# Kernel tuning notes

Measured on AMD Instinct MI355X. Metric: run time of the kernel, lower is better.

The kernel has to match this reference:

```python
import jax, jax.numpy as jnp
import numpy as np

N = 100000
E = 3200000
F_IN = 512
H = 16
C = 40


def gcn_conv(x, edge_index, W, b, num_nodes):
    """PyG GCNConv: y = D^{-1/2} (A + I) D^{-1/2} (x @ W) + b.
    edge_index: [2, E] int, row=source, col=target; self-loops added here."""
    # transform first (small hidden dim keeps message traffic low)
    h = x @ W  # [N, out]
    loops = jnp.arange(num_nodes, dtype=edge_index.dtype)
    row = jnp.concatenate([edge_index[0], loops])
    col = jnp.concatenate([edge_index[1], loops])
    deg = jax.ops.segment_sum(jnp.ones_like(col, dtype=h.dtype), col,
                              num_segments=num_nodes)  # in-degree incl. self-loop
    dinv = jnp.where(deg > 0, jax.lax.rsqrt(deg), 0.0)
    norm = dinv[row] * dinv[col]  # [E+N]
    msgs = h[row] * norm[:, None]  # gather + scale, [E+N, out]
    out = jax.ops.segment_sum(msgs, col, num_segments=num_nodes)  # scatter-add
    return out + b


def setup_inputs() -> dict:
    key = jax.random.key(0)
    k1, k2, k3, k4, k5, k6 = jax.random.split(key, 6)
    x = jax.random.normal(k1, (N, F_IN), dtype=jnp.float32)
    edge_index = jax.random.randint(k2, (2, E), 0, N, dtype=jnp.int64)
    s1 = 1.0 / np.sqrt(F_IN)
    s2 = 1.0 / np.sqrt(H)
    W1 = jax.random.uniform(k3, (F_IN, H), jnp.float32, -s1, s1)
    b1 = jnp.zeros((H,), jnp.float32)
    W2 = jax.random.uniform(k4, (H, C), jnp.float32, -s2, s2)
    b2 = jnp.zeros((C,), jnp.float32)
    return {"x": x, "edge_index": edge_index, "W1": W1, "b1": b1,
            "W2": W2, "b2": b2}


def reference(x, edge_index, W1, b1, W2, b2):
    h = gcn_conv(x, edge_index, W1, b1, N)
    h = jax.nn.relu(h)
    # F.dropout(training=self.training): inference mode -> identity
    h = gcn_conv(h, edge_index, W2, b2, N)
    return jax.nn.log_softmax(h, axis=1)
```

## Files before the change

### kernel.cpp

```cpp
#include <hip/hip_runtime.h>

#define NN 100000
#define EE 3200000
#define FIN 512
#define HH 16
#define CC 40

#define SHIFT 9
#define BNODES 512
#define NB 196
#define CAP 20480
#define CH 2048
#define TC ((EE + CH - 1) / CH)
#define GB ((NN * 4 + 255) / 256)
#define GB2 ((NN + 63) / 64)

__device__ __forceinline__ float bf2f(unsigned short u) {
    return __uint_as_float(((unsigned)u) << 16);
}
__device__ __forceinline__ unsigned short f2bf(float f) {
    unsigned b = __float_as_uint(f);
    return (unsigned short)((b + 0x7FFF + ((b >> 16) & 1)) >> 16);
}

__global__ void k_bin(const int* __restrict__ ei, int* __restrict__ head,
                      unsigned* __restrict__ pairs) {
    __shared__ int h[NB];
    __shared__ int gbase[NB];
    __shared__ int lhead[NB];
    __shared__ int is64_s;
    int t = threadIdx.x;
    if (t < 64) {
        int nz = (ei[2 * t + 1] != 0) ? 1 : 0;
        unsigned long long m = __ballot(nz);
        if (t == 0) is64_s = (m == 0ULL) ? 1 : 0;
    }
    for (int i = t; i < NB; i += 256) { h[i] = 0; lhead[i] = 0; }
    __syncthreads();
    int is64 = is64_s;
    int e0 = blockIdx.x * CH;
    unsigned es[8], ed[8];
#pragma unroll
    for (int j = 0; j < 8; ++j) {
        int e = e0 + j * 256 + t;
        if (e < EE) {
            es[j] = (unsigned)(is64 ? ei[2 * e] : ei[e]);
            ed[j] = (unsigned)(is64 ? ei[2 * (EE + e)] : ei[EE + e]);
            atomicAdd(&h[ed[j] >> SHIFT], 1);
        }
    }
    __syncthreads();
    for (int i = t; i < NB; i += 256)
        gbase[i] = h[i] ? atomicAdd(&head[i], h[i]) : 0;
    __syncthreads();
#pragma unroll
    for (int j = 0; j < 8; ++j) {
        int e = e0 + j * 256 + t;
        if (e < EE) {
            int b = (int)(ed[j] >> SHIFT);
            int p = gbase[b] + atomicAdd(&lhead[b], 1);
            pairs[(size_t)b * CAP + p] = ((ed[j] & (BNODES - 1)) << 17) | es[j];
        }
    }
}

__global__ void __launch_bounds__(256) k_buildgemm(
        const unsigned* __restrict__ pairs, const int* __restrict__ head,
        int* __restrict__ ptr, int* __restrict__ pend,
        float* __restrict__ dinv, int* __restrict__ srcs,
        const float* __restrict__ x, const float* __restrict__ W1,
        float* __restrict__ g1f) {
    __shared__ float red[4][64][17];
    int t = threadIdx.x;
    if (blockIdx.x < NB) {
        int* h   = (int*)red;
        int* lex = (int*)red + BNODES;
        int* wsm = (int*)red + 2 * BNODES;
        int b = blockIdx.x, lane = t & 63, wid = t >> 6;
        int node0 = b << SHIFT;
        int p0 = b * CAP;
        int cnt = head[b];
        for (int i = t; i < BNODES; i += 256) h[i] = 0;
        __syncthreads();
        for (int p = t; p < cnt; p += 256) atomicAdd(&h[pairs[p0 + p] >> 17], 1);
        __syncthreads();
        int a0 = h[2 * t], a1 = h[2 * t + 1];
        int s = a0 + a1;
        int v = s;
#pragma unroll
        for (int off = 1; off < 64; off <<= 1) {
            int u = __shfl_up(v, off);
            if (lane >= off) v += u;
        }
        if (lane == 63) wsm[wid] = v;
        __syncthreads();
        int add = 0;
        for (int w = 0; w < wid; ++w) add += wsm[w];
        int incl = v + add;
        int e0 = incl - s;
        lex[2 * t] = e0;
        lex[2 * t + 1] = e0 + a0;
        __syncthreads();
        for (int i = t; i < BNODES; i += 256) {
            int n = node0 + i;
            if (n < NN) {
                int st = p0 + lex[i];
                ptr[n] = st;
                pend[n] = st + h[i];
                dinv[n] = rsqrtf((float)(h[i] + 1));
            }
        }
        __syncthreads();
        for (int p = t; p < cnt; p += 256) {
            unsigned w = pairs[p0 + p];
            int pos = p0 + atomicAdd(&lex[w >> 17], 1);
            srcs[pos] = (int)(w & 0x1FFFF);
        }
    } else {
        int kq = __builtin_amdgcn_readfirstlane(t >> 6);
        int n = t & 63;
        int base = (blockIdx.x - NB) * 64;
        int nc = min(base + n, NN - 1);
        const float4* xr = reinterpret_cast<const float4*>(
            x + (size_t)nc * FIN + kq * 128);
        const float* wb = W1 + kq * 128 * HH;
        float acc[HH];
#pragma unroll
        for (int f = 0; f < HH; ++f) acc[f] = 0.f;
#pragma unroll 2
        for (int i = 0; i < 32; ++i) {
            float4 xv = xr[i];
            const float* wr = wb + i * 4 * HH;
#pragma unroll
            for (int f = 0; f < HH; ++f) acc[f] = fmaf(xv.x, wr[f], acc[f]);
#pragma unroll
            for (int f = 0; f < HH; ++f) acc[f] = fmaf(xv.y, wr[HH + f], acc[f]);
#pragma unroll
            for (int f = 0; f < HH; ++f) acc[f] = fmaf(xv.z, wr[2 * HH + f], acc[f]);
#pragma unroll
            for (int f = 0; f < HH; ++f) acc[f] = fmaf(xv.w, wr[3 * HH + f], acc[f]);
        }
#pragma unroll
        for (int f = 0; f < HH; ++f) red[kq][n][f] = acc[f];
        __syncthreads();
        int g = t >> 6;
        int f0 = g * 4;
        float r0 = red[0][n][f0]     + red[1][n][f0]     + red[2][n][f0]     + red[3][n][f0];
        float r1 = red[0][n][f0 + 1] + red[1][n][f0 + 1] + red[2][n][f0 + 1] + red[3][n][f0 + 1];
        float r2 = red[0][n][f0 + 2] + red[1][n][f0 + 2] + red[2][n][f0 + 2] + red[3][n][f0 + 2];
        float r3 = red[0][n][f0 + 3] + red[1][n][f0 + 3] + red[2][n][f0 + 3] + red[3][n][f0 + 3];
        int node = base + n;
        if (node < NN)
            reinterpret_cast<float4*>(g1f)[node * 4 + g] =
                make_float4(r0, r1, r2, r3);
    }
}

__global__ void k_scale(const float* __restrict__ g1f, const float* __restrict__ dinv,
                        unsigned short* __restrict__ g1) {
    int gt = blockIdx.x * 256 + threadIdx.x;
    int node = gt >> 2, q = gt & 3;
    if (node >= NN) return;
    float di = dinv[node];
    float4 v = reinterpret_cast<const float4*>(g1f)[node * 4 + q];
    ushort4 o;
    o.x = f2bf(v.x * di);
    o.y = f2bf(v.y * di);
    o.z = f2bf(v.z * di);
    o.w = f2bf(v.w * di);
    reinterpret_cast<ushort4*>(g1)[node * 4 + q] = o;
}

__global__ void k_agg1(const unsigned short* __restrict__ g1, const int* __restrict__ ptr,
                       const int* __restrict__ pend, const int* __restrict__ srcs,
                       const float* __restrict__ dinv, const float* __restrict__ b1,
                       unsigned short* __restrict__ g2h) {
    int gt = blockIdx.x * blockDim.x + threadIdx.x;
    int node = gt >> 2, q = gt & 3;
    if (node >= NN) return;
    const ushort4* G = reinterpret_cast<const ushort4*>(g1);
    ushort4 sv = G[node * 4 + q];
    float ax = bf2f(sv.x), ay = bf2f(sv.y), az = bf2f(sv.z), aw = bf2f(sv.w);
    float bx = 0.f, by = 0.f, bz = 0.f, bw = 0.f;
    float cx = 0.f, cy = 0.f, cz = 0.f, cw = 0.f;
    float dx = 0.f, dy = 0.f, dz = 0.f, dw = 0.f;
    int e = ptr[node], e1 = pend[node];
    for (; e + 3 < e1; e += 4) {
        int s0 = srcs[e], s1 = srcs[e + 1], s2 = srcs[e + 2], s3 = srcs[e + 3];
        ushort4 v0 = G[s0 * 4 + q];
        ushort4 v1 = G[s1 * 4 + q];
        ushort4 v2 = G[s2 * 4 + q];
        ushort4 v3 = G[s3 * 4 + q];
        ax += bf2f(v0.x); ay += bf2f(v0.y); az += bf2f(v0.z); aw += bf2f(v0.w);
        bx += bf2f(v1.x); by += bf2f(v1.y); bz += bf2f(v1.z); bw += bf2f(v1.w);
        cx += bf2f(v2.x); cy += bf2f(v2.y); cz += bf2f(v2.z); cw += bf2f(v2.w);
        dx += bf2f(v3.x); dy += bf2f(v3.y); dz += bf2f(v3.z); dw += bf2f(v3.w);
    }
    for (; e < e1; ++e) {
        ushort4 v = G[srcs[e] * 4 + q];
        ax += bf2f(v.x); ay += bf2f(v.y); az += bf2f(v.z); aw += bf2f(v.w);
    }
    ax += bx + cx + dx;
    ay += by + cy + dy;
    az += bz + cz + dz;
    aw += bw + cw + dw;
    float di = dinv[node];
    const float4 bb = reinterpret_cast<const float4*>(b1)[q];
    ushort4 r;
    r.x = f2bf(fmaxf(fmaf(di, ax, bb.x), 0.f) * di);
    r.y = f2bf(fmaxf(fmaf(di, ay, bb.y), 0.f) * di);
    r.z = f2bf(fmaxf(fmaf(di, az, bb.z), 0.f) * di);
    r.w = f2bf(fmaxf(fmaf(di, aw, bb.w), 0.f) * di);
    reinterpret_cast<ushort4*>(g2h)[node * 4 + q] = r;
}

__global__ void __launch_bounds__(256) k_agg2out(
        const unsigned short* __restrict__ g2h, const int* __restrict__ ptr,
        const int* __restrict__ pend, const int* __restrict__ srcs,
        const float* __restrict__ dinv, const float* __restrict__ W2,
        const float* __restrict__ b2, float* __restrict__ out) {
    __shared__ float w2s[HH * 41];
    __shared__ float b2s[CC];
    int t = threadIdx.x;
    for (int i = t; i < HH * CC; i += 256) w2s[(i / CC) * 41 + (i % CC)] = W2[i];
    if (t < CC) b2s[t] = b2[t];
    __syncthreads();
    int gt = blockIdx.x * blockDim.x + t;
    int node = gt >> 2, q = gt & 3;
    if (node >= NN) return;
    const ushort4* G = reinterpret_cast<const ushort4*>(g2h);
    ushort4 sv = G[node * 4 + q];
    float ax = bf2f(sv.x), ay = bf2f(sv.y), az = bf2f(sv.z), aw = bf2f(sv.w);
    float bx = 0.f, by = 0.f, bz = 0.f, bw = 0.f;
    float cx = 0.f, cy = 0.f, cz = 0.f, cw = 0.f;
    float dx = 0.f, dy = 0.f, dz = 0.f, dw = 0.f;
    int e = ptr[node], e1 = pend[node];
    for (; e + 3 < e1; e += 4) {
        int s0 = srcs[e], s1 = srcs[e + 1], s2 = srcs[e + 2], s3 = srcs[e + 3];
        ushort4 v0 = G[s0 * 4 + q];
        ushort4 v1 = G[s1 * 4 + q];
        ushort4 v2 = G[s2 * 4 + q];
        ushort4 v3 = G[s3 * 4 + q];
        ax += bf2f(v0.x); ay += bf2f(v0.y); az += bf2f(v0.z); aw += bf2f(v0.w);
        bx += bf2f(v1.x); by += bf2f(v1.y); bz += bf2f(v1.z); bw += bf2f(v1.w);
        cx += bf2f(v2.x); cy += bf2f(v2.y); cz += bf2f(v2.z); cw += bf2f(v2.w);
        dx += bf2f(v3.x); dy += bf2f(v3.y); dz += bf2f(v3.z); dw += bf2f(v3.w);
    }
    for (; e < e1; ++e) {
        ushort4 v = G[srcs[e] * 4 + q];
        ax += bf2f(v.x); ay += bf2f(v.y); az += bf2f(v.z); aw += bf2f(v.w);
    }
    ax += bx + cx + dx;
    ay += by + cy + dy;
    az += bz + cz + dz;
    aw += bw + cw + dw;
    const float* w0 = w2s + (4 * q + 0) * 41;
    const float* w1 = w2s + (4 * q + 1) * 41;
    const float* w2r = w2s + (4 * q + 2) * 41;
    const float* w3 = w2s + (4 * q + 3) * 41;
    float y[CC];
#pragma unroll
    for (int c = 0; c < CC; ++c)
        y[c] = fmaf(ax, w0[c], fmaf(ay, w1[c], fmaf(az, w2r[c], aw * w3[c])));
#pragma unroll
    for (int c = 0; c < CC; ++c) {
        y[c] += __shfl_xor(y[c], 1);
        y[c] += __shfl_xor(y[c], 2);
    }
    float di = dinv[node];
    float m = -3.0e38f;
#pragma unroll
    for (int c = 0; c < CC; ++c) {
        y[c] = fmaf(di, y[c], b2s[c]);
        m = fmaxf(m, y[c]);
    }
    float ssum = 0.f;
#pragma unroll
    for (int c = 0; c < CC; ++c) ssum += expf(y[c] - m);
    float l = logf(ssum) + m;
    float ov[10];
#pragma unroll
    for (int c = 0; c < CC; ++c) {
        if ((c / 10) == q) ov[c % 10] = y[c] - l;
    }
    float2* o2 = reinterpret_cast<float2*>(out + (size_t)node * CC + 10 * q);
#pragma unroll
    for (int i = 0; i < 5; ++i) o2[i] = make_float2(ov[2 * i], ov[2 * i + 1]);
}

extern "C" void kernel_launch(void* const* d_in, const int* in_sizes, int n_in,
                              void* d_out, int out_size, void* d_ws, size_t ws_size,
                              hipStream_t stream) {
    const float* x  = (const float*)d_in[0];
    const int*   ei = (const int*)d_in[1];
    const float* W1 = (const float*)d_in[2];
    const float* b1 = (const float*)d_in[3];
    const float* W2 = (const float*)d_in[4];
    const float* b2 = (const float*)d_in[5];
    float* out = (float*)d_out;

    char* w = (char*)d_ws;
    auto alloc = [&](size_t bytes) {
        char* p = w;
        w += (bytes + 255) & ~(size_t)255;
        return p;
    };
    int*            head  = (int*)alloc((size_t)NB * 4);
    int*            ptr   = (int*)alloc((size_t)NN * 4);
    int*            pend  = (int*)alloc((size_t)NN * 4);
    float*          dinv  = (float*)alloc((size_t)NN * 4);
    unsigned*       pairs = (unsigned*)alloc((size_t)NB * CAP * 4);
    int*            srcs  = (int*)alloc((size_t)NB * CAP * 4);
    float*          g1f   = (float*)alloc((size_t)NN * HH * 4);
    unsigned short* g1    = (unsigned short*)alloc((size_t)NN * HH * 2);
    unsigned short* g2h   = (unsigned short*)alloc((size_t)NN * HH * 2);

    hipMemsetAsync(head, 0, (size_t)NB * sizeof(int), stream);
    k_bin<<<TC, 256, 0, stream>>>(ei, head, pairs);
    k_buildgemm<<<NB + GB2, 256, 0, stream>>>(pairs, head, ptr, pend, dinv, srcs,
                                              x, W1, g1f);
    k_scale<<<GB, 256, 0, stream>>>(g1f, dinv, g1);
    int nt = NN * 4;
    k_agg1<<<(nt + 255) / 256, 256, 0, stream>>>(g1, ptr, pend, srcs, dinv, b1, g2h);
    k_agg2out<<<(nt + 255) / 256, 256, 0, stream>>>(g2h, ptr, pend, srcs, dinv,
                                                    W2, b2, out);
}
```

Measured before the change: 468.3 us.

## Stage x tiles through double-buffered swizzled LDS for coalesced GEMM loads

The x@W1 part of the fused build/GEMM kernel now loads x rows cooperatively and coalesced: eight lanes read 128 contiguous bytes of a row. The rows go into a double-buffered, XOR-swizzled shared-memory tile. Each wave then computes 4 output features for all 64 nodes, so the cross-wave LDS reduction of partial sums goes away. Previously each lane streamed its own row with strided float4 loads. The change adds a barrier per chunk and needs more LDS traffic, but it targets the uncoalesced global reads of the 200 MB x matrix.

```diff
diff --git a/kernel.cpp b/kernel.cpp
--- a/kernel.cpp
+++ b/kernel.cpp
@@ -70,12 +70,12 @@
         float* __restrict__ dinv, int* __restrict__ srcs,
         const float* __restrict__ x, const float* __restrict__ W1,
         float* __restrict__ g1f) {
-    __shared__ float red[4][64][17];
+    __shared__ float xs[2][64][32];
     int t = threadIdx.x;
     if (blockIdx.x < NB) {
-        int* h   = (int*)red;
-        int* lex = (int*)red + BNODES;
-        int* wsm = (int*)red + 2 * BNODES;
+        int* h   = (int*)xs;
+        int* lex = (int*)xs + BNODES;
+        int* wsm = (int*)xs + 2 * BNODES;
         int b = blockIdx.x, lane = t & 63, wid = t >> 6;
         int node0 = b << SHIFT;
         int p0 = b * CAP;
@@ -117,42 +117,63 @@
             srcs[pos] = (int)(w & 0x1FFFF);
         }
     } else {
-        int kq = __builtin_amdgcn_readfirstlane(t >> 6);
-        int n = t & 63;
+        int w = __builtin_amdgcn_readfirstlane(t >> 6);
+        int lane = t & 63;
+        int ln7 = lane & 7;
         int base = (blockIdx.x - NB) * 64;
-        int nc = min(base + n, NN - 1);
-        const float4* xr = reinterpret_cast<const float4*>(
-            x + (size_t)nc * FIN + kq * 128);
-        const float* wb = W1 + kq * 128 * HH;
-        float acc[HH];
-#pragma unroll
-        for (int f = 0; f < HH; ++f) acc[f] = 0.f;
-#pragma unroll 2
-        for (int i = 0; i < 32; ++i) {
-            float4 xv = xr[i];
-            const float* wr = wb + i * 4 * HH;
-#pragma unroll
-            for (int f = 0; f < HH; ++f) acc[f] = fmaf(xv.x, wr[f], acc[f]);
-#pragma unroll
-            for (int f = 0; f < HH; ++f) acc[f] = fmaf(xv.y, wr[HH + f], acc[f]);
-#pragma unroll
-            for (int f = 0; f < HH; ++f) acc[f] = fmaf(xv.z, wr[2 * HH + f], acc[f]);
-#pragma unroll
-            for (int f = 0; f < HH; ++f) acc[f] = fmaf(xv.w, wr[3 * HH + f], acc[f]);
-        }
-#pragma unroll
-        for (int f = 0; f < HH; ++f) red[kq][n][f] = acc[f];
-        __syncthreads();
-        int g = t >> 6;
-        int f0 = g * 4;
-        float r0 = red[0][n][f0]     + red[1][n][f0]     + red[2][n][f0]     + red[3][n][f0];
-        float r1 = red[0][n][f0 + 1] + red[1][n][f0 + 1] + red[2][n][f0 + 1] + red[3][n][f0 + 1];
-        float r2 = red[0][n][f0 + 2] + red[1][n][f0 + 2] + red[2][n][f0 + 2] + red[3][n][f0 + 2];
-        float r3 = red[0][n][f0 + 3] + red[1][n][f0 + 3] + red[2][n][f0 + 3] + red[3][n][f0 + 3];
-        int node = base + n;
+        int r0 = w * 16 + (lane >> 3);
+        int r1 = r0 + 8;
+        const float* src0 = x + (size_t)min(base + r0, NN - 1) * FIN + ln7 * 4;
+        const float* src1 = x + (size_t)min(base + r1, NN - 1) * FIN + ln7 * 4;
+        int c0 = (ln7 ^ (r0 & 7)) * 4;
+        int c1 = (ln7 ^ (r1 & 7)) * 4;
+        const float* wq = W1 + w * 4;
+        float4 acc = make_float4(0.f, 0.f, 0.f, 0.f);
+        {
+            float4 v0 = *(const float4*)(src0);
+            float4 v1 = *(const float4*)(src1);
+            *(float4*)&xs[0][r0][c0] = v0;
+            *(float4*)&xs[0][r1][c1] = v1;
+        }
+        __syncthreads();
+#pragma unroll 4
+        for (int ch = 0; ch < 16; ++ch) {
+            int cb = ch & 1;
+            float4 n0, n1;
+            if (ch < 15) {
+                n0 = *(const float4*)(src0 + (ch + 1) * 32);
+                n1 = *(const float4*)(src1 + (ch + 1) * 32);
+            }
+#pragma unroll
+            for (int s = 0; s < 8; ++s) {
+                float4 xv = *(const float4*)&xs[cb][lane][(s ^ ln7) * 4];
+                const float* wr = wq + (ch * 32 + s * 4) * HH;
+                acc.x = fmaf(xv.x, wr[0], acc.x);
+                acc.y = fmaf(xv.x, wr[1], acc.y);
+                acc.z = fmaf(xv.x, wr[2], acc.z);
+                acc.w = fmaf(xv.x, wr[3], acc.w);
+                acc.x = fmaf(xv.y, wr[HH + 0], acc.x);
+                acc.y = fmaf(xv.y, wr[HH + 1], acc.y);
+                acc.z = fmaf(xv.y, wr[HH + 2], acc.z);
+                acc.w = fmaf(xv.y, wr[HH + 3], acc.w);
+                acc.x = fmaf(xv.z, wr[2 * HH + 0], acc.x);
+                acc.y = fmaf(xv.z, wr[2 * HH + 1], acc.y);
+                acc.z = fmaf(xv.z, wr[2 * HH + 2], acc.z);
+                acc.w = fmaf(xv.z, wr[2 * HH + 3], acc.w);
+                acc.x = fmaf(xv.w, wr[3 * HH + 0], acc.x);
+                acc.y = fmaf(xv.w, wr[3 * HH + 1], acc.y);
+                acc.z = fmaf(xv.w, wr[3 * HH + 2], acc.z);
+                acc.w = fmaf(xv.w, wr[3 * HH + 3], acc.w);
+            }
+            if (ch < 15) {
+                *(float4*)&xs[cb ^ 1][r0][c0] = n0;
+                *(float4*)&xs[cb ^ 1][r1][c1] = n1;
+            }
+            __syncthreads();
+        }
+        int node = base + lane;
         if (node < NN)
-            reinterpret_cast<float4*>(g1f)[node * 4 + g] =
-                make_float4(r0, r1, r2, r3);
+            reinterpret_cast<float4*>(g1f)[node * 4 + w] = acc;
     }
 }
 
```

Result: slower. 491.2 us (+4.9%).
